# Optimization experiments

Hardware: AMD Instinct MI355X
Metric: run time of the kernel (lower is better)

Reference implementation:

```python
import jax, jax.numpy as jnp
import numpy as np


def setup_inputs() -> dict:
    key = jax.random.key(0)
    kx, kt = jax.random.split(key)
    b, n, d = 4, 4096, 1024
    x = jax.random.normal(kx, (b, n, d), dtype=jnp.float32)
    t = jax.random.normal(kt, (n, d), dtype=jnp.float32)
    return {"x": x, "t": t}


def reference(x, t):
    # y[b,i,d] = sum_{j<=i} t[i-j,d] * x[b,j,d]
    # Causal depthwise Toeplitz matvec == linear convolution truncated to n.
    # Computed via FFT along the sequence axis (zero-pad to 2n so the
    # circular convolution equals the linear one on the first n outputs).
    b, n, d = x.shape
    L = 2 * n
    xf = jnp.fft.rfft(x.astype(jnp.float32), n=L, axis=1)        # (b, L/2+1, d) complex
    tf = jnp.fft.rfft(t.astype(jnp.float32), n=L, axis=0)        # (L/2+1, d) complex
    y = jnp.fft.irfft(xf * tf[None], n=L, axis=1)[:, :n, :]      # (b, n, d)
    return y.astype(x.dtype)
```

## Files before the change

kernel.cpp:

```cpp
#include <hip/hip_runtime.h>

#define NT 512
#define SCL (1.0f / 8192.0f)
#define PI_F 3.14159265358979323846f

__device__ __forceinline__ int P(int i) { return i ^ ((i >> 5) & 31); }

__device__ __forceinline__ float2 cmul(float2 a, float2 b) {
  return make_float2(a.x * b.x - a.y * b.y, a.x * b.y + a.y * b.x);
}
__device__ __forceinline__ float2 csqr(float2 a) {
  return make_float2(a.x * a.x - a.y * a.y, 2.f * a.x * a.y);
}
__device__ __forceinline__ float2 cadd(float2 a, float2 b) { return make_float2(a.x + b.x, a.y + b.y); }
__device__ __forceinline__ float2 csub(float2 a, float2 b) { return make_float2(a.x - b.x, a.y - b.y); }
__device__ __forceinline__ float2 cmuli (float2 a) { return make_float2(-a.y,  a.x); }
__device__ __forceinline__ float2 cmulmi(float2 a) { return make_float2( a.y, -a.x); }

constexpr float RT2 = 0.70710678118654752440f;
constexpr float CQ1 = 0.92387953251128675613f;
constexpr float SQ1 = 0.38268343236508977173f;
constexpr float C8x[4] = {1.f,  RT2, 0.f, -RT2};
constexpr float C8y[4] = {0.f, -RT2, -1.f, -RT2};
constexpr float C16x[8] = {1.f,  CQ1,  RT2,  SQ1, 0.f, -SQ1, -RT2, -CQ1};
constexpr float C16y[8] = {0.f, -SQ1, -RT2, -CQ1, -1.f, -CQ1, -RT2, -SQ1};

template<bool UNIT>
__device__ __forceinline__ void r8_fwd(float2* e, float2 b) {
  float2 b2, b4;
  if (!UNIT) { b2 = csqr(b); b4 = csqr(b2); }
  #pragma unroll
  for (int j = 0; j < 4; ++j) {
    float2 u = e[j], v = e[j + 4];
    float2 d = csub(u, v);
    e[j] = cadd(u, v);
    float2 c8 = make_float2(C8x[j], C8y[j]);
    if (UNIT) e[j + 4] = (j == 0) ? d : cmul(d, c8);
    else      e[j + 4] = cmul(d, (j == 0) ? b : cmul(b, c8));
  }
  #pragma unroll
  for (int o = 0; o < 8; o += 4) {
    #pragma unroll
    for (int j = 0; j < 2; ++j) {
      float2 u = e[o + j], v = e[o + j + 2];
      float2 d = csub(u, v);
      e[o + j] = cadd(u, v);
      if (UNIT) e[o + j + 2] = (j == 0) ? d : cmulmi(d);
      else      e[o + j + 2] = cmul(d, (j == 0) ? b2 : cmulmi(b2));
    }
  }
  #pragma unroll
  for (int o = 0; o < 8; o += 2) {
    float2 u = e[o], v = e[o + 1];
    float2 d = csub(u, v);
    e[o] = cadd(u, v);
    e[o + 1] = UNIT ? d : cmul(d, b4);
  }
}

template<bool UNIT>
__device__ __forceinline__ void r8_inv(float2* e, float2 g) {
  float2 g2, g4;
  if (!UNIT) { g2 = csqr(g); g4 = csqr(g2); }
  #pragma unroll
  for (int o = 0; o < 8; o += 2) {
    float2 t = UNIT ? e[o + 1] : cmul(e[o + 1], g4);
    float2 u = e[o];
    e[o] = cadd(u, t); e[o + 1] = csub(u, t);
  }
  #pragma unroll
  for (int o = 0; o < 8; o += 4) {
    #pragma unroll
    for (int j = 0; j < 2; ++j) {
      float2 v = e[o + j + 2];
      float2 t;
      if (UNIT) t = (j == 0) ? v : cmuli(v);
      else      t = cmul(v, (j == 0) ? g2 : cmuli(g2));
      float2 u = e[o + j];
      e[o + j] = cadd(u, t); e[o + j + 2] = csub(u, t);
    }
  }
  #pragma unroll
  for (int j = 0; j < 4; ++j) {
    float2 v = e[j + 4];
    float2 t;
    float2 c8c = make_float2(C8x[j], -C8y[j]);
    if (UNIT) t = (j == 0) ? v : cmul(v, c8c);
    else      t = cmul(v, (j == 0) ? g : cmul(g, c8c));
    float2 u = e[j];
    e[j] = cadd(u, t); e[j + 4] = csub(u, t);
  }
}

__device__ __forceinline__ void t8f(float2* cb, int base, int G, float2 b) {
  float2 e[8];
  #pragma unroll
  for (int j = 0; j < 8; ++j) e[j] = cb[P(base + G * j)];
  r8_fwd<false>(e, b);
  #pragma unroll
  for (int j = 0; j < 8; ++j) cb[P(base + G * j)] = e[j];
}

__device__ __forceinline__ void t8i(float2* cb, int base, int G, float2 g) {
  float2 e[8];
  #pragma unroll
  for (int j = 0; j < 8; ++j) e[j] = cb[P(base + G * j)];
  r8_inv<false>(e, g);
  #pragma unroll
  for (int j = 0; j < 8; ++j) cb[P(base + G * j)] = e[j];
}

__global__ __launch_bounds__(NT)
void that8h(const float* __restrict__ tT, float2* __restrict__ ThG) {
  __shared__ float2 cb[4096];
  const int tid = threadIdx.x;
  const int d = blockIdx.x;
  const int half = blockIdx.y;

  const int baseB = ((tid >> 6) << 9) + (tid & 63);
  const int baseC = ((tid >> 3) << 6) + (tid & 7);

  float s0, c0; __sincosf(-PI_F * (float)tid / 2048.f, &s0, &c0);
  const float2 bA = make_float2(c0, s0);
  float s1, c1; __sincosf(-PI_F * (float)(tid & 63) / 256.f, &s1, &c1);
  const float2 bB = make_float2(c1, s1);
  float s2, c2; __sincosf(-PI_F * (float)(tid & 7) / 32.f, &s2, &c2);
  const float2 bC = make_float2(c2, s2);
  float sw, cw; __sincosf(-PI_F * (float)tid / 4096.f, &sw, &cw);
  const float2 whi = make_float2(cw, sw);

  const float* tp = tT + (size_t)d * 4096;
  {
    float2 e[8];
    #pragma unroll
    for (int j = 0; j < 8; ++j) {
      int n = tid + 512 * j;
      float tv = tp[n];
      if (half == 0) e[j] = make_float2(tv, 0.f);
      else {
        float2 w = (j == 0) ? whi : cmul(whi, make_float2(C16x[j], C16y[j]));
        e[j] = make_float2(tv * w.x, tv * w.y);
      }
    }
    r8_fwd<false>(e, bA);
    #pragma unroll
    for (int j = 0; j < 8; ++j) cb[P(tid + 512 * j)] = e[j];
  }
  __syncthreads();
  t8f(cb, baseB, 64, bB);  __syncthreads();
  t8f(cb, baseC, 8, bC);   __syncthreads();
  float2* thg = ThG + ((size_t)d * 2 + half) * 4096;
  float2 e[8];
  #pragma unroll
  for (int j = 0; j < 8; ++j) e[j] = cb[P(tid * 8 + j)];
  r8_fwd<true>(e, make_float2(1.f, 0.f));
  #pragma unroll
  for (int j = 0; j < 8; ++j)
    thg[tid + 512 * j] = make_float2(e[j].x * SCL, e[j].y * SCL);
}

__global__ __launch_bounds__(NT)
void fftconv(float* __restrict__ xT, const float2* __restrict__ ThG) {
  __shared__ float2 cb[4096];
  const int tid = threadIdx.x;
  const int d = blockIdx.x;
  const int pass = blockIdx.y;

  const int baseB = ((tid >> 6) << 9) + (tid & 63);
  const int baseC = ((tid >> 3) << 6) + (tid & 7);
  const int baseM = tid << 3;
  const float2 ONE = make_float2(1.f, 0.f);

  float s0, c0; __sincosf(-PI_F * (float)tid / 2048.f, &s0, &c0);
  const float2 bA = make_float2(c0, s0);
  const float2 gA = make_float2(c0, -s0);
  float s1, c1; __sincosf(-PI_F * (float)(tid & 63) / 256.f, &s1, &c1);
  const float2 bB = make_float2(c1, s1);
  const float2 gB = make_float2(c1, -s1);
  float s2, c2; __sincosf(-PI_F * (float)(tid & 7) / 32.f, &s2, &c2);
  const float2 bC = make_float2(c2, s2);
  const float2 gC = make_float2(c2, -s2);
  float sw, cw; __sincosf(-PI_F * (float)tid / 4096.f, &sw, &cw);
  const float2 whi  = make_float2(cw, sw);
  const float2 whic = make_float2(cw, -sw);

  float* r0 = xT + ((size_t)(2 * pass)     * 1024 + d) * 4096;
  float* r1 = xT + ((size_t)(2 * pass + 1) * 1024 + d) * 4096;
  const float2* thl = ThG + (size_t)d * 2 * 4096;
  const float2* thh = thl + 4096;

  float2 u[8];
  float2 th[8];

  {
    float2 e[8];
    #pragma unroll
    for (int j = 0; j < 8; ++j) {
      int n = tid + 512 * j;
      e[j] = make_float2(r0[n], r1[n]);
    }
    r8_fwd<false>(e, bA);
    #pragma unroll
    for (int j = 0; j < 8; ++j) cb[P(tid + 512 * j)] = e[j];
  }
  __syncthreads();
  t8f(cb, baseB, 64, bB);  __syncthreads();
  #pragma unroll
  for (int j = 0; j < 8; ++j) th[j] = thl[tid + 512 * j];
  t8f(cb, baseC, 8, bC);   __syncthreads();
  {
    float2 e[8];
    #pragma unroll
    for (int j = 0; j < 8; ++j) e[j] = cb[P(baseM + j)];
    r8_fwd<true>(e, ONE);
    #pragma unroll
    for (int j = 0; j < 8; ++j) e[j] = cmul(e[j], th[j]);
    r8_inv<true>(e, ONE);
    #pragma unroll
    for (int j = 0; j < 8; ++j) cb[P(baseM + j)] = e[j];
  }
  __syncthreads();
  t8i(cb, baseC, 8, gC);   __syncthreads();
  t8i(cb, baseB, 64, gB);  __syncthreads();
  #pragma unroll
  for (int j = 0; j < 8; ++j) u[j] = cb[P(tid + 512 * j)];
  r8_inv<false>(u, gA);
  __syncthreads();

  {
    float2 e[8];
    #pragma unroll
    for (int j = 0; j < 8; ++j) {
      int n = tid + 512 * j;
      float2 xv = make_float2(r0[n], r1[n]);
      float2 w = (j == 0) ? whi : cmul(whi, make_float2(C16x[j], C16y[j]));
      e[j] = cmul(xv, w);
    }
    r8_fwd<false>(e, bA);
    #pragma unroll
    for (int j = 0; j < 8; ++j) cb[P(tid + 512 * j)] = e[j];
  }
  __syncthreads();
  t8f(cb, baseB, 64, bB);  __syncthreads();
  #pragma unroll
  for (int j = 0; j < 8; ++j) th[j] = thh[tid + 512 * j];
  t8f(cb, baseC, 8, bC);   __syncthreads();
  {
    float2 e[8];
    #pragma unroll
    for (int j = 0; j < 8; ++j) e[j] = cb[P(baseM + j)];
    r8_fwd<true>(e, ONE);
    #pragma unroll
    for (int j = 0; j < 8; ++j) e[j] = cmul(e[j], th[j]);
    r8_inv<true>(e, ONE);
    #pragma unroll
    for (int j = 0; j < 8; ++j) cb[P(baseM + j)] = e[j];
  }
  __syncthreads();
  t8i(cb, baseC, 8, gC);   __syncthreads();
  t8i(cb, baseB, 64, gB);  __syncthreads();
  {
    float2 v[8];
    #pragma unroll
    for (int j = 0; j < 8; ++j) v[j] = cb[P(tid + 512 * j)];
    r8_inv<false>(v, gA);
    #pragma unroll
    for (int k = 0; k < 8; ++k) {
      float2 wc = (k == 0) ? whic : cmul(whic, make_float2(C16x[k], -C16y[k]));
      float2 t = cmul(v[k], wc);
      int n = tid + 512 * k;
      r0[n] = u[k].x + t.x;
      r1[n] = u[k].y + t.y;
    }
  }
}

__global__ __launch_bounds__(256)
void transpose64(const float* __restrict__ src, float* __restrict__ dst, int R, int C) {
  __shared__ float tile[64][65];
  int t  = threadIdx.x;
  int c4 = t & 15;
  int r  = t >> 4;
  size_t slab = (size_t)blockIdx.z * (size_t)R * (size_t)C;
  const float* s = src + slab;
  float* dd = dst + slab;
  int col0 = blockIdx.x * 64, row0 = blockIdx.y * 64;
  #pragma unroll
  for (int k = 0; k < 4; ++k) {
    int rr = r + 16 * k;
    const float4 v = *(const float4*)(s + (size_t)(row0 + rr) * C + col0 + 4 * c4);
    tile[rr][4 * c4 + 0] = v.x;
    tile[rr][4 * c4 + 1] = v.y;
    tile[rr][4 * c4 + 2] = v.z;
    tile[rr][4 * c4 + 3] = v.w;
  }
  __syncthreads();
  #pragma unroll
  for (int k = 0; k < 4; ++k) {
    int cc = r + 16 * k;
    float4 w;
    w.x = tile[4 * c4 + 0][cc];
    w.y = tile[4 * c4 + 1][cc];
    w.z = tile[4 * c4 + 2][cc];
    w.w = tile[4 * c4 + 3][cc];
    *(float4*)(dd + (size_t)(col0 + cc) * R + row0 + 4 * c4) = w;
  }
}

extern "C" void kernel_launch(void* const* d_in, const int* in_sizes, int n_in,
                              void* d_out, int out_size, void* d_ws, size_t ws_size,
                              hipStream_t stream) {
  const float* x = (const float*)d_in[0];
  const float* t = (const float*)d_in[1];
  float* out = (float*)d_out;
  float* ws  = (float*)d_ws;
  float* xT  = ws;
  float* tT  = ws + (size_t)4 * 1024 * 4096;
  float2* ThG = (float2*)d_out;

  transpose64<<<dim3(16, 64, 4), 256, 0, stream>>>(x, xT, 4096, 1024);
  transpose64<<<dim3(16, 64, 1), 256, 0, stream>>>(t, tT, 4096, 1024);

  that8h<<<dim3(1024, 2), NT, 0, stream>>>(tT, ThG);
  fftconv<<<dim3(1024, 2), NT, 0, stream>>>(xT, ThG);

  transpose64<<<dim3(64, 16, 4), 256, 0, stream>>>(xT, out, 1024, 4096);
}
```

Baseline: 153.8 us.

## Fuse last two radix-8 FFT stages via wavefront shuffle transpose instead of LDS

The last forward radix-8 stage (baseC) and the innermost stage are merged into a single register pass. An 8x8 in-register transpose across lanes, built from xor shuffles, replaces the LDS round-trip and barrier that used to sit between them. The same is done on the inverse side, so each half pass drops two shared-memory write/read rounds and two __syncthreads. The precompute kernel gets the same fusion. The spectral multiplier loads are also hoisted earlier to overlap with the B stage. The cost is extra shuffle instructions and register pressure, and correctness depends on the transpose matching the previous index mapping.

```diff
diff --git a/kernel.cpp b/kernel.cpp
--- a/kernel.cpp
+++ b/kernel.cpp
@@ -92,6 +92,23 @@
   }
 }
 
+__device__ __forceinline__ void xpose8(float2* e, int tid) {
+  #pragma unroll
+  for (int m = 1; m < 8; m <<= 1) {
+    #pragma unroll
+    for (int r = 0; r < 8; ++r) {
+      if ((r & m) == 0) {
+        const bool hi = (tid & m) != 0;
+        float2 a = hi ? e[r] : e[r | m];
+        float2 b;
+        b.x = __shfl_xor(a.x, m, 64);
+        b.y = __shfl_xor(a.y, m, 64);
+        if (hi) e[r] = b; else e[r | m] = b;
+      }
+    }
+  }
+}
+
 __device__ __forceinline__ void t8f(float2* cb, int base, int G, float2 b) {
   float2 e[8];
   #pragma unroll
@@ -148,15 +165,18 @@
   }
   __syncthreads();
   t8f(cb, baseB, 64, bB);  __syncthreads();
-  t8f(cb, baseC, 8, bC);   __syncthreads();
-  float2* thg = ThG + ((size_t)d * 2 + half) * 4096;
-  float2 e[8];
-  #pragma unroll
-  for (int j = 0; j < 8; ++j) e[j] = cb[P(tid * 8 + j)];
-  r8_fwd<true>(e, make_float2(1.f, 0.f));
-  #pragma unroll
-  for (int j = 0; j < 8; ++j)
-    thg[tid + 512 * j] = make_float2(e[j].x * SCL, e[j].y * SCL);
+  {
+    float2 e[8];
+    #pragma unroll
+    for (int j = 0; j < 8; ++j) e[j] = cb[P(baseC + 8 * j)];
+    r8_fwd<false>(e, bC);
+    xpose8(e, tid);
+    r8_fwd<true>(e, make_float2(1.f, 0.f));
+    float2* thg = ThG + ((size_t)d * 2 + half) * 4096;
+    #pragma unroll
+    for (int j = 0; j < 8; ++j)
+      thg[tid + 512 * j] = make_float2(e[j].x * SCL, e[j].y * SCL);
+  }
 }
 
 __global__ __launch_bounds__(NT)
@@ -168,7 +188,6 @@
 
   const int baseB = ((tid >> 6) << 9) + (tid & 63);
   const int baseC = ((tid >> 3) << 6) + (tid & 7);
-  const int baseM = tid << 3;
   const float2 ONE = make_float2(1.f, 0.f);
 
   float s0, c0; __sincosf(-PI_F * (float)tid / 2048.f, &s0, &c0);
@@ -204,23 +223,25 @@
     for (int j = 0; j < 8; ++j) cb[P(tid + 512 * j)] = e[j];
   }
   __syncthreads();
+  #pragma unroll
+  for (int j = 0; j < 8; ++j) th[j] = thl[tid + 512 * j];
   t8f(cb, baseB, 64, bB);  __syncthreads();
-  #pragma unroll
-  for (int j = 0; j < 8; ++j) th[j] = thl[tid + 512 * j];
-  t8f(cb, baseC, 8, bC);   __syncthreads();
-  {
-    float2 e[8];
-    #pragma unroll
-    for (int j = 0; j < 8; ++j) e[j] = cb[P(baseM + j)];
+  {
+    float2 e[8];
+    #pragma unroll
+    for (int j = 0; j < 8; ++j) e[j] = cb[P(baseC + 8 * j)];
+    r8_fwd<false>(e, bC);
+    xpose8(e, tid);
     r8_fwd<true>(e, ONE);
     #pragma unroll
     for (int j = 0; j < 8; ++j) e[j] = cmul(e[j], th[j]);
     r8_inv<true>(e, ONE);
-    #pragma unroll
-    for (int j = 0; j < 8; ++j) cb[P(baseM + j)] = e[j];
-  }
-  __syncthreads();
-  t8i(cb, baseC, 8, gC);   __syncthreads();
+    xpose8(e, tid);
+    r8_inv<false>(e, gC);
+    #pragma unroll
+    for (int j = 0; j < 8; ++j) cb[P(baseC + 8 * j)] = e[j];
+  }
+  __syncthreads();
   t8i(cb, baseB, 64, gB);  __syncthreads();
   #pragma unroll
   for (int j = 0; j < 8; ++j) u[j] = cb[P(tid + 512 * j)];
@@ -241,23 +262,25 @@
     for (int j = 0; j < 8; ++j) cb[P(tid + 512 * j)] = e[j];
   }
   __syncthreads();
+  #pragma unroll
+  for (int j = 0; j < 8; ++j) th[j] = thh[tid + 512 * j];
   t8f(cb, baseB, 64, bB);  __syncthreads();
-  #pragma unroll
-  for (int j = 0; j < 8; ++j) th[j] = thh[tid + 512 * j];
-  t8f(cb, baseC, 8, bC);   __syncthreads();
-  {
-    float2 e[8];
-    #pragma unroll
-    for (int j = 0; j < 8; ++j) e[j] = cb[P(baseM + j)];
+  {
+    float2 e[8];
+    #pragma unroll
+    for (int j = 0; j < 8; ++j) e[j] = cb[P(baseC + 8 * j)];
+    r8_fwd<false>(e, bC);
+    xpose8(e, tid);
     r8_fwd<true>(e, ONE);
     #pragma unroll
     for (int j = 0; j < 8; ++j) e[j] = cmul(e[j], th[j]);
     r8_inv<true>(e, ONE);
-    #pragma unroll
-    for (int j = 0; j < 8; ++j) cb[P(baseM + j)] = e[j];
-  }
-  __syncthreads();
-  t8i(cb, baseC, 8, gC);   __syncthreads();
+    xpose8(e, tid);
+    r8_inv<false>(e, gC);
+    #pragma unroll
+    for (int j = 0; j < 8; ++j) cb[P(baseC + 8 * j)] = e[j];
+  }
+  __syncthreads();
   t8i(cb, baseB, 64, gB);  __syncthreads();
   {
     float2 v[8];
```

Measured after the change: 314.4 us. 2.04x slower.

## Process both half-spectrum FFTs together in one block with doubled shared buffer

Applied to the files above, without the earlier changes.

Both kernels now run the low and high (twisted) half FFTs side by side in a 64 KB shared buffer instead of one after the other. Each pass applies to both halves between barriers, which roughly halves the number of __syncthreads and removes the second global read of x. that8h merges its two half blocks into one, reading t once. Doubling LDS per block and holding both twiddle sets in registers may reduce occupancy.

```diff
diff --git a/kernel.cpp b/kernel.cpp
--- a/kernel.cpp
+++ b/kernel.cpp
@@ -112,10 +112,9 @@
 
 __global__ __launch_bounds__(NT)
 void that8h(const float* __restrict__ tT, float2* __restrict__ ThG) {
-  __shared__ float2 cb[4096];
+  __shared__ float2 cb[8192];
   const int tid = threadIdx.x;
   const int d = blockIdx.x;
-  const int half = blockIdx.y;
 
   const int baseB = ((tid >> 6) << 9) + (tid & 63);
   const int baseC = ((tid >> 3) << 6) + (tid & 7);
@@ -131,37 +130,47 @@
 
   const float* tp = tT + (size_t)d * 4096;
   {
+    float2 tv[8];
+    #pragma unroll
+    for (int j = 0; j < 8; ++j) tv[j] = make_float2(tp[tid + 512 * j], 0.f);
     float2 e[8];
     #pragma unroll
+    for (int j = 0; j < 8; ++j) e[j] = tv[j];
+    r8_fwd<false>(e, bA);
+    #pragma unroll
+    for (int j = 0; j < 8; ++j) cb[P(tid + 512 * j)] = e[j];
+    #pragma unroll
     for (int j = 0; j < 8; ++j) {
-      int n = tid + 512 * j;
-      float tv = tp[n];
-      if (half == 0) e[j] = make_float2(tv, 0.f);
-      else {
-        float2 w = (j == 0) ? whi : cmul(whi, make_float2(C16x[j], C16y[j]));
-        e[j] = make_float2(tv * w.x, tv * w.y);
-      }
+      float2 w = (j == 0) ? whi : cmul(whi, make_float2(C16x[j], C16y[j]));
+      e[j] = make_float2(tv[j].x * w.x, tv[j].x * w.y);
     }
     r8_fwd<false>(e, bA);
     #pragma unroll
-    for (int j = 0; j < 8; ++j) cb[P(tid + 512 * j)] = e[j];
-  }
-  __syncthreads();
-  t8f(cb, baseB, 64, bB);  __syncthreads();
-  t8f(cb, baseC, 8, bC);   __syncthreads();
-  float2* thg = ThG + ((size_t)d * 2 + half) * 4096;
-  float2 e[8];
-  #pragma unroll
-  for (int j = 0; j < 8; ++j) e[j] = cb[P(tid * 8 + j)];
-  r8_fwd<true>(e, make_float2(1.f, 0.f));
-  #pragma unroll
-  for (int j = 0; j < 8; ++j)
-    thg[tid + 512 * j] = make_float2(e[j].x * SCL, e[j].y * SCL);
+    for (int j = 0; j < 8; ++j) cb[P(4096 + tid + 512 * j)] = e[j];
+  }
+  __syncthreads();
+  t8f(cb, baseB, 64, bB);
+  t8f(cb, 4096 + baseB, 64, bB);
+  __syncthreads();
+  t8f(cb, baseC, 8, bC);
+  t8f(cb, 4096 + baseC, 8, bC);
+  __syncthreads();
+  float2* thg = ThG + (size_t)d * 2 * 4096;
+  #pragma unroll 1
+  for (int h = 0; h < 2; ++h) {
+    float2 e[8];
+    #pragma unroll
+    for (int j = 0; j < 8; ++j) e[j] = cb[P(h * 4096 + tid * 8 + j)];
+    r8_fwd<true>(e, make_float2(1.f, 0.f));
+    #pragma unroll
+    for (int j = 0; j < 8; ++j)
+      thg[h * 4096 + tid + 512 * j] = make_float2(e[j].x * SCL, e[j].y * SCL);
+  }
 }
 
 __global__ __launch_bounds__(NT)
 void fftconv(float* __restrict__ xT, const float2* __restrict__ ThG) {
-  __shared__ float2 cb[4096];
+  __shared__ float2 cb[8192];
   const int tid = threadIdx.x;
   const int d = blockIdx.x;
   const int pass = blockIdx.y;
@@ -189,80 +198,72 @@
   const float2* thl = ThG + (size_t)d * 2 * 4096;
   const float2* thh = thl + 4096;
 
-  float2 u[8];
-  float2 th[8];
-
   {
-    float2 e[8];
+    float2 xv[8];
     #pragma unroll
     for (int j = 0; j < 8; ++j) {
       int n = tid + 512 * j;
-      e[j] = make_float2(r0[n], r1[n]);
-    }
+      xv[j] = make_float2(r0[n], r1[n]);
+    }
+    float2 e[8];
+    #pragma unroll
+    for (int j = 0; j < 8; ++j) e[j] = xv[j];
     r8_fwd<false>(e, bA);
     #pragma unroll
     for (int j = 0; j < 8; ++j) cb[P(tid + 512 * j)] = e[j];
-  }
-  __syncthreads();
-  t8f(cb, baseB, 64, bB);  __syncthreads();
-  #pragma unroll
-  for (int j = 0; j < 8; ++j) th[j] = thl[tid + 512 * j];
-  t8f(cb, baseC, 8, bC);   __syncthreads();
+    #pragma unroll
+    for (int j = 0; j < 8; ++j) {
+      float2 w = (j == 0) ? whi : cmul(whi, make_float2(C16x[j], C16y[j]));
+      e[j] = cmul(xv[j], w);
+    }
+    r8_fwd<false>(e, bA);
+    #pragma unroll
+    for (int j = 0; j < 8; ++j) cb[P(4096 + tid + 512 * j)] = e[j];
+  }
+  __syncthreads();
+
+  float2 thL[8], thH[8];
+  #pragma unroll
+  for (int j = 0; j < 8; ++j) thL[j] = thl[tid + 512 * j];
+  #pragma unroll
+  for (int j = 0; j < 8; ++j) thH[j] = thh[tid + 512 * j];
+  t8f(cb, baseB, 64, bB);
+  t8f(cb, 4096 + baseB, 64, bB);
+  __syncthreads();
+
+  t8f(cb, baseC, 8, bC);
+  t8f(cb, 4096 + baseC, 8, bC);
+  __syncthreads();
+
+  #pragma unroll 1
+  for (int h = 0; h < 2; ++h) {
+    float2 e[8];
+    #pragma unroll
+    for (int j = 0; j < 8; ++j) e[j] = cb[P(h * 4096 + baseM + j)];
+    r8_fwd<true>(e, ONE);
+    #pragma unroll
+    for (int j = 0; j < 8; ++j) e[j] = cmul(e[j], h ? thH[j] : thL[j]);
+    r8_inv<true>(e, ONE);
+    #pragma unroll
+    for (int j = 0; j < 8; ++j) cb[P(h * 4096 + baseM + j)] = e[j];
+  }
+  __syncthreads();
+
+  t8i(cb, baseC, 8, gC);
+  t8i(cb, 4096 + baseC, 8, gC);
+  __syncthreads();
+
+  t8i(cb, baseB, 64, gB);
+  t8i(cb, 4096 + baseB, 64, gB);
+  __syncthreads();
+
   {
-    float2 e[8];
-    #pragma unroll
-    for (int j = 0; j < 8; ++j) e[j] = cb[P(baseM + j)];
-    r8_fwd<true>(e, ONE);
-    #pragma unroll
-    for (int j = 0; j < 8; ++j) e[j] = cmul(e[j], th[j]);
-    r8_inv<true>(e, ONE);
-    #pragma unroll
-    for (int j = 0; j < 8; ++j) cb[P(baseM + j)] = e[j];
-  }
-  __syncthreads();
-  t8i(cb, baseC, 8, gC);   __syncthreads();
-  t8i(cb, baseB, 64, gB);  __syncthreads();
-  #pragma unroll
-  for (int j = 0; j < 8; ++j) u[j] = cb[P(tid + 512 * j)];
-  r8_inv<false>(u, gA);
-  __syncthreads();
-
-  {
-    float2 e[8];
-    #pragma unroll
-    for (int j = 0; j < 8; ++j) {
-      int n = tid + 512 * j;
-      float2 xv = make_float2(r0[n], r1[n]);
-      float2 w = (j == 0) ? whi : cmul(whi, make_float2(C16x[j], C16y[j]));
-      e[j] = cmul(xv, w);
-    }
-    r8_fwd<false>(e, bA);
-    #pragma unroll
-    for (int j = 0; j < 8; ++j) cb[P(tid + 512 * j)] = e[j];
-  }
-  __syncthreads();
-  t8f(cb, baseB, 64, bB);  __syncthreads();
-  #pragma unroll
-  for (int j = 0; j < 8; ++j) th[j] = thh[tid + 512 * j];
-  t8f(cb, baseC, 8, bC);   __syncthreads();
-  {
-    float2 e[8];
-    #pragma unroll
-    for (int j = 0; j < 8; ++j) e[j] = cb[P(baseM + j)];
-    r8_fwd<true>(e, ONE);
-    #pragma unroll
-    for (int j = 0; j < 8; ++j) e[j] = cmul(e[j], th[j]);
-    r8_inv<true>(e, ONE);
-    #pragma unroll
-    for (int j = 0; j < 8; ++j) cb[P(baseM + j)] = e[j];
-  }
-  __syncthreads();
-  t8i(cb, baseC, 8, gC);   __syncthreads();
-  t8i(cb, baseB, 64, gB);  __syncthreads();
-  {
-    float2 v[8];
-    #pragma unroll
-    for (int j = 0; j < 8; ++j) v[j] = cb[P(tid + 512 * j)];
+    float2 u[8], v[8];
+    #pragma unroll
+    for (int j = 0; j < 8; ++j) u[j] = cb[P(tid + 512 * j)];
+    r8_inv<false>(u, gA);
+    #pragma unroll
+    for (int j = 0; j < 8; ++j) v[j] = cb[P(4096 + tid + 512 * j)];
     r8_inv<false>(v, gA);
     #pragma unroll
     for (int k = 0; k < 8; ++k) {
@@ -321,7 +322,7 @@
   transpose64<<<dim3(16, 64, 4), 256, 0, stream>>>(x, xT, 4096, 1024);
   transpose64<<<dim3(16, 64, 1), 256, 0, stream>>>(t, tT, 4096, 1024);
 
-  that8h<<<dim3(1024, 2), NT, 0, stream>>>(tT, ThG);
+  that8h<<<dim3(1024), NT, 0, stream>>>(tT, ThG);
   fftconv<<<dim3(1024, 2), NT, 0, stream>>>(xT, ThG);
 
   transpose64<<<dim3(64, 16, 4), 256, 0, stream>>>(xT, out, 1024, 4096);
```

Measured after the change: 152.5 us. No clear change (-0.8%).
